# Kernel optimization log

Measured on AMD Instinct MI355X. Metric: run time of the kernel, lower is better.

## Reference

```python
import jax, jax.numpy as jnp
import numpy as np

D_STATE = 16
D_CONV = 4

def layernorm(x, g, b, eps=1e-5):
    m = jnp.mean(x, -1, keepdims=True)
    v = jnp.var(x, -1, keepdims=True)
    return (x - m) / jnp.sqrt(v + eps) * g + b

def conv1x1(x, w):  # x [b,h,w,cin], w [cin,cout]
    return jnp.einsum('bhwc,cd->bhwd', x, w)

def dwconv3x3(x, w):  # x [b,h,w,C], w [3,3,1,C] (HWIO, groups=C)
    return jax.lax.conv_general_dilated(x, w, (1, 1), 'SAME',
        dimension_numbers=('NHWC', 'HWIO', 'NHWC'),
        feature_group_count=x.shape[-1])

def causal_dwconv1d(x, w, b):  # x [B,L,D], w [K,1,D]; causal depthwise conv (Mamba d_conv=4)
    xp = jnp.pad(x, ((0, 0), (D_CONV - 1, 0), (0, 0)))
    y = jax.lax.conv_general_dilated(xp, w, (1,), 'VALID',
        dimension_numbers=('NWC', 'WIO', 'NWC'),
        feature_group_count=x.shape[-1])
    return y + b

def selective_scan(deltaA, deltaBx, C):
    # deltaA, deltaBx: [B,L,D,S]; C: [B,L,S] -> y: [B,L,D]
    def step(h, inp):
        dA, dBx, c = inp
        h = dA * h + dBx
        return h, jnp.einsum('bds,bs->bd', h, c)
    h0 = jnp.zeros(deltaA.shape[:1] + deltaA.shape[2:], deltaA.dtype)
    _, ys = jax.lax.scan(step, h0,
        (jnp.swapaxes(deltaA, 0, 1), jnp.swapaxes(deltaBx, 0, 1), jnp.swapaxes(C, 0, 1)))
    return jnp.swapaxes(ys, 0, 1)

def spa_ssm(x, in_w, conv_w, conv_b, xproj_w, dt_w, dt_b, Alog, D, out_w):
    # Mamba (slow path) applied to flattened spatial sequence; x: [b,h,w,c]
    b, h, w, c = x.shape
    L = h * w
    xs = x.reshape(b, L, c)
    di = Alog.shape[0]
    xz = xs @ in_w                       # [b,L,2*di]
    xi, z = xz[..., :di], xz[..., di:]
    xi = jax.nn.silu(causal_dwconv1d(xi, conv_w, conv_b))
    dbc = xi @ xproj_w                   # [b,L,dt_rank+2*S]
    dtr = dt_w.shape[0]
    dt = jax.nn.softplus(dbc[..., :dtr] @ dt_w + dt_b)   # [b,L,di]
    B = dbc[..., dtr:dtr + D_STATE]
    C = dbc[..., dtr + D_STATE:]
    A = -jnp.exp(Alog)                   # [di,S]
    deltaA = jnp.exp(dt[..., None] * A)                  # [b,L,di,S]
    deltaBx = (dt * xi)[..., None] * B[:, :, None, :]    # [b,L,di,S]
    y = selective_scan(deltaA, deltaBx, C) + D * xi
    y = y * jax.nn.silu(z)
    return (y @ out_w).reshape(b, h, w, c)

def camba_forward(x, ln1_g, ln1_b, vin_w1, vin_dw, vin_w2, vout_dw1, vout_dw2,
                  ssm_in_w, ssm_conv_w, ssm_conv_b, ssm_xproj_w, ssm_dt_w, ssm_dt_b,
                  ssm_Alog, ssm_D, ssm_out_w, ln2_g, ln2_b, ff_w1, ff_dw, ff_w2):
    x = jnp.transpose(x, (0, 2, 3, 1))   # [b,h,w,c]
    # ESSM: v_in_head = LN -> 1x1 -> dw3x3 -> GELU -> 1x1
    x0 = conv1x1(layernorm(x, ln1_g, ln1_b), vin_w1)
    x0 = jax.nn.gelu(dwconv3x3(x0, vin_dw), approximate=False)
    x0 = conv1x1(x0, vin_w2)
    y = spa_ssm(x0, ssm_in_w, ssm_conv_w, ssm_conv_b, ssm_xproj_w,
                ssm_dt_w, ssm_dt_b, ssm_Alog, ssm_D, ssm_out_w) + x0
    # v_out_head = dw3x3 -> GELU -> dw3x3, residual
    y = dwconv3x3(jax.nn.gelu(dwconv3x3(y, vout_dw1), approximate=False), vout_dw2) + y
    x = y + x                            # block residual
    # PreNorm FeedForward (mult=4): 1x1 -> LReLU -> dw3x3 -> LReLU -> 1x1
    t = layernorm(x, ln2_g, ln2_b)
    t = jax.nn.leaky_relu(conv1x1(t, ff_w1), 0.2)
    t = jax.nn.leaky_relu(dwconv3x3(t, ff_dw), 0.2)
    t = conv1x1(t, ff_w2)
    x = t + x
    return jnp.transpose(x, (0, 3, 1, 2))

def setup_inputs() -> dict:
    key = jax.random.key(0)
    ks = jax.random.split(key, 16)
    b, c, h, w = 8, 64, 64, 64
    di, ds, dtr = 128, 16, 4
    s = 0.05
    n = lambda k, shp: jax.random.normal(k, shp, jnp.float32) * s
    dt0 = jnp.exp(jax.random.uniform(ks[1], (di,)) * (np.log(0.1) - np.log(1e-3)) + np.log(1e-3))
    return dict(
        x=jax.random.normal(ks[0], (b, c, h, w), jnp.float32),
        ln1_g=jnp.ones(c), ln1_b=jnp.zeros(c),
        vin_w1=n(ks[2], (c, c)), vin_dw=n(ks[3], (3, 3, 1, c)), vin_w2=n(ks[4], (c, c)),
        vout_dw1=n(ks[5], (3, 3, 1, c)), vout_dw2=n(ks[6], (3, 3, 1, c)),
        ssm_in_w=n(ks[7], (c, 2 * di)),
        ssm_conv_w=n(ks[8], (D_CONV, 1, di)), ssm_conv_b=jnp.zeros(di),
        ssm_xproj_w=n(ks[9], (di, dtr + 2 * ds)),
        ssm_dt_w=n(ks[10], (dtr, di)), ssm_dt_b=jnp.log(jnp.expm1(dt0)),
        ssm_Alog=jnp.log(jnp.broadcast_to(jnp.arange(1., ds + 1), (di, ds))),
        ssm_D=jnp.ones(di),
        ssm_out_w=n(ks[11], (di, c)),
        ln2_g=jnp.ones(c), ln2_b=jnp.zeros(c),
        ff_w1=n(ks[12], (c, 4 * c)), ff_dw=n(ks[13], (3, 3, 1, 4 * c)), ff_w2=n(ks[14], (4 * c, c)),
    )

def reference(x, ln1_g, ln1_b, vin_w1, vin_dw, vin_w2, vout_dw1, vout_dw2,
              ssm_in_w, ssm_conv_w, ssm_conv_b, ssm_xproj_w, ssm_dt_w, ssm_dt_b,
              ssm_Alog, ssm_D, ssm_out_w, ln2_g, ln2_b, ff_w1, ff_dw, ff_w2):
    return camba_forward(x, ln1_g, ln1_b, vin_w1, vin_dw, vin_w2, vout_dw1, vout_dw2,
                         ssm_in_w, ssm_conv_w, ssm_conv_b, ssm_xproj_w, ssm_dt_w, ssm_dt_b,
                         ssm_Alog, ssm_D, ssm_out_w, ln2_g, ln2_b, ff_w1, ff_dw, ff_w2)
```

## Files before the change

### kernel.cpp

```cpp
#include <hip/hip_runtime.h>
#include <hip/hip_bf16.h>
#include <math.h>

typedef unsigned short u16;
typedef __attribute__((ext_vector_type(8))) short s8v;
typedef __attribute__((ext_vector_type(4))) float f4v;

#define B_    8
#define C_    64
#define HW_   4096
#define NPIX  32768
#define DI    128
#define NCH   256
#define CHL   16

__device__ __forceinline__ float b2f(u16 v){ return __uint_as_float(((unsigned)v)<<16); }
__device__ __forceinline__ u16 f2b(float x){
  unsigned u = __float_as_uint(x);
  u += 0x7fff + ((u >> 16) & 1);
  return (u16)(u >> 16);
}
__device__ __forceinline__ float gelu_exact(float x){ return 0.5f*x*(1.0f+erff(x*0.70710678118654752f)); }
__device__ __forceinline__ float leaky02(float x){ return x>0.f ? x : 0.2f*x; }
__device__ __forceinline__ float softplus_(float x){ return fmaxf(x,0.f)+log1pf(__expf(-fabsf(x))); }
__device__ __forceinline__ float silu_(float x){ return x / (1.0f + __expf(-x)); }
__device__ __forceinline__ void unpack16(uint4 q0, uint4 q1, float* v){
  unsigned w[8]={q0.x,q0.y,q0.z,q0.w,q1.x,q1.y,q1.z,q1.w};
  #pragma unroll
  for(int j=0;j<8;j++){
    v[2*j]   = __uint_as_float(w[j]<<16);
    v[2*j+1] = __uint_as_float(w[j]&0xffff0000u);
  }
}

__global__ void k_prep(const float* __restrict__ vin_w1, const float* __restrict__ vin_w2,
                       const float* __restrict__ ssm_in_w, const float* __restrict__ xproj,
                       const float* __restrict__ dtw, const float* __restrict__ ssm_outw,
                       const float* __restrict__ ff_w1, const float* __restrict__ ff_w2,
                       u16* __restrict__ wv1, u16* __restrict__ wv2, u16* __restrict__ wsi,
                       u16* __restrict__ wdb, u16* __restrict__ wout, u16* __restrict__ wf1,
                       u16* __restrict__ wf2t){
  int g = blockIdx.x*256 + threadIdx.x;
  if(g < 4096){
    int n=g>>6, c=g&63;
    wv1[n*64+c]=f2b(vin_w1[c*64+n]);
    wv2[n*64+c]=f2b(vin_w2[c*64+n]);
  }
  if(g < 16384){
    int n=g>>6, c=g&63;
    wsi[n*64+c]=f2b(ssm_in_w[c*256+n]);
    wf1[n*64+c]=f2b(ff_w1[c*256+n]);
    int n2=g/256, k2=g%256;
    wf2t[n2*256+k2]=f2b(ff_w2[k2*64+n2]);
  }
  if(g < 8192){
    int n=g>>7, k=g&127;
    wout[n*128+k]=f2b(ssm_outw[k*64+n]);
  }
  if(g < 20480){
    int n=g/128, k=g%128;
    float v;
    if(n < 128){
      v = 0.f;
      for(int r=0;r<4;r++) v += xproj[k*36+r]*dtw[r*128+n];
    }else{
      v = xproj[k*36+4+(n-128)];
    }
    wdb[n*128+k]=f2b(v);
  }
}

__global__ __launch_bounds__(256) void k_trans_ln_mm(const float* __restrict__ x,
                     const float* __restrict__ g, const float* __restrict__ bta,
                     const u16* __restrict__ wT,
                     u16* __restrict__ xT, u16* __restrict__ outp){
  const int LDA = 72, NS = 4;
  __shared__ float tile[64][65];
  __shared__ __align__(16) u16 sA[64*LDA];
  __shared__ __align__(16) u16 sW[64*LDA];
  int tid = threadIdx.x;
  int blk = blockIdx.x;
  int b = blk >> 6;
  int hwb = (blk & 63) << 6;
  int lane = tid & 63, row = tid >> 6;
  const float* src = x + (size_t)b*C_*HW_;
  #pragma unroll
  for(int k=0;k<16;k++){
    int c = row + 4*k;
    tile[c][lane] = src[c*HW_ + hwb + lane];
  }
  for(int idx=tid; idx<64*8; idx+=256){
    int n = idx>>3, c8 = (idx&7)*8;
    *(uint4*)(sW + n*LDA + c8) = *(const uint4*)(wT + n*64 + c8);
  }
  __syncthreads();
  u16* dstT = xT + (size_t)b*HW_*C_;
  #pragma unroll
  for(int k=0;k<16;k++){
    int hwl = row + 4*k;
    dstT[(hwb+hwl)*C_ + lane] = f2b(tile[lane][hwl]);
  }
  float gg = g[lane], bb = bta[lane];
  #pragma unroll
  for(int i=0;i<16;i++){
    int hwl = row*16 + i;
    float v = tile[lane][hwl];
    float s = v, sq = v*v;
    #pragma unroll
    for(int o=32;o>0;o>>=1){ s += __shfl_xor(s,o); sq += __shfl_xor(sq,o); }
    float m = s*(1.f/64.f);
    float var = sq*(1.f/64.f) - m*m;
    float r = rsqrtf(var + 1e-5f);
    sA[hwl*LDA + lane] = f2b((v-m)*r*gg + bb);
  }
  __syncthreads();
  int ln = tid & 63, wv = tid >> 6;
  int mrow = ln & 15, quad = ln >> 4;
  f4v acc[NS];
  #pragma unroll
  for(int i=0;i<NS;i++) acc[i] = (f4v){0.f,0.f,0.f,0.f};
  const u16* aBase = sA + (wv*16 + mrow)*LDA + quad*8;
  const u16* wBase = sW + mrow*LDA + quad*8;
  #pragma unroll
  for(int kk=0; kk<64; kk+=32){
    s8v af = *(const s8v*)(aBase + kk);
    #pragma unroll
    for(int ns=0; ns<NS; ns++){
      s8v bf = *(const s8v*)(wBase + ns*16*LDA + kk);
      acc[ns] = __builtin_amdgcn_mfma_f32_16x16x32_bf16(af, bf, acc[ns], 0, 0, 0);
    }
  }
  int p0 = blk*64;
  int pr = p0 + wv*16 + quad*4;
  #pragma unroll
  for(int ns=0; ns<NS; ns++){
    int n = ns*16 + mrow;
    #pragma unroll
    for(int r=0;r<4;r++)
      outp[(size_t)(pr+r)*64 + n] = f2b(acc[ns][r]);
  }
}

__global__ __launch_bounds__(256) void k_dw3mm(const u16* __restrict__ in,
                     const float* __restrict__ dwgt, const u16* __restrict__ wT,
                     u16* __restrict__ x0){
  const int LDT = 72;
  __shared__ __align__(16) u16 sIn[10*10*64];
  __shared__ __align__(16) u16 sT[64*LDT];
  __shared__ __align__(16) u16 sW[64*LDT];
  int tid = threadIdx.x;
  int blk = blockIdx.x;
  int b = blk >> 6;
  int t6 = blk & 63;
  int h0 = (t6 >> 3) * 8, w0 = (t6 & 7) * 8;
  for(int idx=tid; idx<64*8; idx+=256){
    int n = idx>>3, c8 = (idx&7)*8;
    *(uint4*)(sW + n*LDT + c8) = *(const uint4*)(wT + n*64 + c8);
  }
  for(int q=tid; q<10*10*16; q+=256){
    int pp = q >> 4, c4 = q & 15;
    int hh = pp / 10, ww = pp % 10;
    int gh = h0-1+hh, gw = w0-1+ww;
    ushort4 v = make_ushort4(0,0,0,0);
    if((unsigned)gh < 64u && (unsigned)gw < 64u)
      v = *(const ushort4*)(in + (size_t)((b*64+gh)*64+gw)*64 + c4*4);
    *(ushort4*)(sIn + pp*64 + c4*4) = v;
  }
  __syncthreads();
  int c4 = tid & 15;
  #pragma unroll
  for(int pass=0; pass<4; pass++){
    int opix = pass*16 + (tid>>4);
    int oh = opix >> 3, ow = opix & 7;
    float a0=0.f,a1=0.f,a2=0.f,a3=0.f;
    #pragma unroll
    for(int kh=0;kh<3;kh++){
      #pragma unroll
      for(int kw=0;kw<3;kw++){
        ushort4 v = *(const ushort4*)(sIn + ((oh+kh)*10 + (ow+kw))*64 + c4*4);
        float4 wv = *(const float4*)(dwgt + (kh*3+kw)*64 + c4*4);
        a0 += b2f(v.x)*wv.x; a1 += b2f(v.y)*wv.y;
        a2 += b2f(v.z)*wv.z; a3 += b2f(v.w)*wv.w;
      }
    }
    ushort4 o; o.x=f2b(gelu_exact(a0)); o.y=f2b(gelu_exact(a1));
    o.z=f2b(gelu_exact(a2)); o.w=f2b(gelu_exact(a3));
    *(ushort4*)(sT + opix*LDT + c4*4) = o;
  }
  __syncthreads();
  int ln = tid & 63, wv = tid >> 6;
  int mrow = ln & 15, quad = ln >> 4;
  f4v acc[4];
  #pragma unroll
  for(int i=0;i<4;i++) acc[i] = (f4v){0.f,0.f,0.f,0.f};
  const u16* aBase = sT + (wv*16 + mrow)*LDT + quad*8;
  const u16* wBase = sW + mrow*LDT + quad*8;
  #pragma unroll
  for(int kk=0; kk<64; kk+=32){
    s8v af = *(const s8v*)(aBase + kk);
    #pragma unroll
    for(int ns=0; ns<4; ns++){
      s8v bf = *(const s8v*)(wBase + ns*16*LDT + kk);
      acc[ns] = __builtin_amdgcn_mfma_f32_16x16x32_bf16(af, bf, acc[ns], 0, 0, 0);
    }
  }
  #pragma unroll
  for(int ns=0; ns<4; ns++){
    int n = ns*16 + mrow;
    #pragma unroll
    for(int r=0;r<4;r++){
      int opix = wv*16 + quad*4 + r;
      int oh = opix >> 3, ow = opix & 7;
      size_t p = ((size_t)(b*64 + h0+oh)*64 + (w0+ow));
      x0[p*64 + n] = f2b(acc[ns][r]);
    }
  }
}

template<int CIN, int COUT, int ACT, bool OUTF32>
__global__ __launch_bounds__(256) void k_mfma(const u16* __restrict__ wT,
                     const u16* __restrict__ in, const float* __restrict__ bias,
                     const u16* __restrict__ res, void* __restrict__ outv){
  const int KCH = (CIN < 128) ? CIN : 128;
  const int LDA = KCH + 8;
  const int NS  = COUT / 16;
  __shared__ __align__(16) u16 sA[64*LDA];
  __shared__ __align__(16) u16 sW[COUT*LDA];
  int tid = threadIdx.x;
  int p0 = blockIdx.x * 64;
  int ln = tid & 63, wv = tid >> 6;
  int mrow = ln & 15, quad = ln >> 4;
  f4v acc[NS];
  #pragma unroll
  for(int i=0;i<NS;i++) acc[i] = (f4v){0.f,0.f,0.f,0.f};
  const u16* aBase = sA + (wv*16 + mrow)*LDA + quad*8;
  const u16* wBase = sW + mrow*LDA + quad*8;
  const int RW = KCH/8;
  for(int k0=0; k0<CIN; k0+=KCH){
    if(k0) __syncthreads();
    for(int idx=tid; idx<COUT*RW; idx+=256){
      int n = idx/RW, c8 = (idx%RW)*8;
      *(uint4*)(sW + n*LDA + c8) = *(const uint4*)(wT + (size_t)n*CIN + k0 + c8);
    }
    for(int g=tid; g<64*RW; g+=256){
      int row = g / RW, c8 = (g % RW)*8;
      *(uint4*)(sA + row*LDA + c8) = *(const uint4*)(in + (size_t)(p0+row)*CIN + k0 + c8);
    }
    __syncthreads();
    #pragma unroll
    for(int kk=0; kk<KCH; kk+=32){
      s8v af = *(const s8v*)(aBase + kk);
      #pragma unroll
      for(int ns=0; ns<NS; ns++){
        s8v bf = *(const s8v*)(wBase + ns*16*LDA + kk);
        acc[ns] = __builtin_amdgcn_mfma_f32_16x16x32_bf16(af, bf, acc[ns], 0, 0, 0);
      }
    }
  }
  int pr = p0 + wv*16 + quad*4;
  #pragma unroll
  for(int ns=0; ns<NS; ns++){
    int n = ns*16 + mrow;
    float bs = bias ? bias[n] : 0.f;
    #pragma unroll
    for(int r=0;r<4;r++){
      float v = acc[ns][r] + bs;
      if(ACT==1) v = leaky02(v);
      else if(ACT==2) v = softplus_(v);
      if(res) v += b2f(res[(size_t)(pr+r)*COUT + n]);
      if(OUTF32) ((float*)outv)[(size_t)(pr+r)*COUT + n] = v;
      else       ((u16*)outv)[(size_t)(pr+r)*COUT + n] = f2b(v);
    }
  }
}

__global__ __launch_bounds__(256) void k_ssm_dtbc(const u16* __restrict__ wT,
                     const u16* __restrict__ x0,
                     const float* __restrict__ cw, const float* __restrict__ cb,
                     const u16* __restrict__ wdb, const float* __restrict__ dtbias,
                     u16* __restrict__ xi, u16* __restrict__ zs,
                     u16* __restrict__ dtout, u16* __restrict__ bcout){
  const int LDA=72, NS=16, LDY=136, LDWD=136, NS2=10;
  __shared__ __align__(16) u16 S[31616];
  u16* sW   = S;
  u16* sA   = S + 18432;
  u16* ubuf = S + 23040;
  u16* xiT  = S;
  u16* wdbS = S + 8704;
  int tid = threadIdx.x;
  int p0 = blockIdx.x*64;
  int ln = tid & 63, wv = tid >> 6;
  int mrow = ln & 15, quad = ln >> 4;
  for(int idx=tid; idx<256*8; idx+=256){
    int n = idx>>3, c8 = (idx&7)*8;
    *(uint4*)(sW + n*LDA + c8) = *(const uint4*)(wT + n*64 + c8);
  }
  for(int g=tid; g<64*8; g+=256){
    int row = g >> 3, c8 = (g & 7)*8;
    *(uint4*)(sA + row*LDA + c8) = *(const uint4*)(x0 + (size_t)(p0+row)*64 + c8);
  }
  __syncthreads();
  f4v acc[NS];
  #pragma unroll
  for(int i=0;i<NS;i++) acc[i] = (f4v){0.f,0.f,0.f,0.f};
  const u16* aBase = sA + (wv*16 + mrow)*LDA + quad*8;
  const u16* wBase = sW + mrow*LDA + quad*8;
  #pragma unroll
  for(int kk=0; kk<64; kk+=32){
    s8v af = *(const s8v*)(aBase + kk);
    #pragma unroll
    for(int ns=0; ns<NS; ns++){
      s8v bf = *(const s8v*)(wBase + ns*16*LDA + kk);
      acc[ns] = __builtin_amdgcn_mfma_f32_16x16x32_bf16(af, bf, acc[ns], 0, 0, 0);
    }
  }
  bool bstart = ((p0 & 4095) == 0);
  for(int idx=tid; idx<384; idx+=256){
    int j = idx >> 7, n = idx & 127;
    float a2 = 0.f;
    if(!bstart){
      const u16* xr = x0 + (size_t)(p0-3+j)*64;
      #pragma unroll 8
      for(int c=0;c<64;c++) a2 += b2f(xr[c]) * b2f(sW[n*LDA+c]);
    }
    ubuf[j*128 + n] = f2b(a2);
  }
  int prl = wv*16 + quad*4;
  #pragma unroll
  for(int ns=0; ns<NS; ns++){
    int n = ns*16 + mrow;
    if(n < 128){
      #pragma unroll
      for(int r=0;r<4;r++) ubuf[(prl+r+3)*128 + n] = f2b(acc[ns][r]);
    }else{
      #pragma unroll
      for(int r=0;r<4;r++) zs[(size_t)(p0+prl+r)*128 + (n-128)] = f2b(silu_(acc[ns][r]));
    }
  }
  __syncthreads();
  int d4 = tid & 31;
  float4 cbv = *(const float4*)(cb + d4*4);
  for(int row = tid >> 5; row < 64; row += 8){
    float a0=cbv.x, a1=cbv.y, a2=cbv.z, a3=cbv.w;
    #pragma unroll
    for(int k=0;k<4;k++){
      ushort4 v = *(const ushort4*)(ubuf + (row+k)*128 + d4*4);
      float4 wv4 = *(const float4*)(cw + k*128 + d4*4);
      a0 += b2f(v.x)*wv4.x; a1 += b2f(v.y)*wv4.y;
      a2 += b2f(v.z)*wv4.z; a3 += b2f(v.w)*wv4.w;
    }
    ushort4 o; o.x=f2b(silu_(a0)); o.y=f2b(silu_(a1)); o.z=f2b(silu_(a2)); o.w=f2b(silu_(a3));
    *(ushort4*)(xi + (size_t)(p0+row)*128 + d4*4) = o;
    *(ushort4*)(xiT + row*LDY + d4*4) = o;
  }
  __syncthreads();
  for(int idx=tid; idx<160*16; idx+=256){
    int n = idx>>4, c8 = (idx&15)*8;
    *(uint4*)(wdbS + n*LDWD + c8) = *(const uint4*)(wdb + n*128 + c8);
  }
  __syncthreads();
  f4v acc2[NS2];
  #pragma unroll
  for(int i=0;i<NS2;i++) acc2[i] = (f4v){0.f,0.f,0.f,0.f};
  #pragma unroll
  for(int kk=0; kk<128; kk+=32){
    s8v af = *(const s8v*)(xiT + (wv*16+mrow)*LDY + kk + quad*8);
    #pragma unroll
    for(int ns=0; ns<NS2; ns++){
      s8v bf = *(const s8v*)(wdbS + (ns*16+mrow)*LDWD + kk + quad*8);
      acc2[ns] = __builtin_amdgcn_mfma_f32_16x16x32_bf16(af, bf, acc2[ns], 0, 0, 0);
    }
  }
  int pr = p0 + wv*16 + quad*4;
  #pragma unroll
  for(int ns=0; ns<NS2; ns++){
    int n = ns*16 + mrow;
    if(n < 128){
      float bs = dtbias[n];
      #pragma unroll
      for(int r=0;r<4;r++)
        dtout[(size_t)(pr+r)*128 + n] = f2b(softplus_(acc2[ns][r] + bs));
    }else{
      #pragma unroll
      for(int r=0;r<4;r++)
        bcout[(size_t)(pr+r)*32 + (n-128)] = f2b(acc2[ns][r]);
    }
  }
}

__global__ __launch_bounds__(256) void k_scan1(const u16* __restrict__ dt, const u16* __restrict__ xi,
                        const u16* __restrict__ bc, const float* __restrict__ alog,
                        u16* __restrict__ Pb, u16* __restrict__ Qb){
  int t = blockIdx.x*256 + threadIdx.x;
  int d = t & 127;
  int ch = (t >> 7) & 255;
  int b = t >> 15;
  int pbase = b*HW_ + ch*CHL;
  float A[16];
  #pragma unroll
  for(int s=0;s<16;s++) A[s] = -__expf(alog[d*16+s]);
  float dtv[16], uv[16];
  #pragma unroll
  for(int i=0;i<CHL;i++){
    dtv[i] = b2f(dt[(size_t)(pbase+i)*128 + d]);
    uv[i]  = dtv[i] * b2f(xi[(size_t)(pbase+i)*128 + d]);
  }
  float Q[16], sumdt = 0.f;
  #pragma unroll
  for(int s=0;s<16;s++) Q[s] = 0.f;
  #pragma unroll
  for(int i=0;i<CHL;i++){
    float Bv[16];
    unpack16(*(const uint4*)(bc + (size_t)(pbase+i)*32),
             *(const uint4*)(bc + (size_t)(pbase+i)*32 + 8), Bv);
    sumdt += dtv[i];
    #pragma unroll
    for(int s=0;s<16;s++){
      float a = __expf(dtv[i]*A[s]);
      Q[s] = a*Q[s] + uv[i]*Bv[s];
    }
  }
  int gidx = ch*16384 + (b*128+d)*16;
  unsigned pw[8], qw[8];
  #pragma unroll
  for(int j=0;j<8;j++){
    pw[j] = (unsigned)f2b(__expf(A[2*j]*sumdt)) | ((unsigned)f2b(__expf(A[2*j+1]*sumdt))<<16);
    qw[j] = (unsigned)f2b(Q[2*j]) | ((unsigned)f2b(Q[2*j+1])<<16);
  }
  *(uint4*)(Pb+gidx)   = make_uint4(pw[0],pw[1],pw[2],pw[3]);
  *(uint4*)(Pb+gidx+8) = make_uint4(pw[4],pw[5],pw[6],pw[7]);
  *(uint4*)(Qb+gidx)   = make_uint4(qw[0],qw[1],qw[2],qw[3]);
  *(uint4*)(Qb+gidx+8) = make_uint4(qw[4],qw[5],qw[6],qw[7]);
}

__global__ __launch_bounds__(256) void k_scan2(const u16* __restrict__ Pb, const u16* __restrict__ Qb,
                        u16* __restrict__ Hin){
  __shared__ __align__(16) u16 sP[256*32];
  __shared__ __align__(16) u16 sQ[256*32];
  __shared__ float gP[8*32];
  __shared__ float gQ[8*32];
  int tid = threadIdx.x;
  int s0 = blockIdx.x * 32;
  for(int idx = tid; idx < 256*4; idx += 256){
    int ch = idx >> 2, j8 = (idx & 3) * 8;
    *(uint4*)(sP + ch*32 + j8) = *(const uint4*)(Pb + (size_t)ch*16384 + s0 + j8);
    *(uint4*)(sQ + ch*32 + j8) = *(const uint4*)(Qb + (size_t)ch*16384 + s0 + j8);
  }
  __syncthreads();
  int sl = tid & 31, grp = tid >> 5;
  int base = grp * 32;
  float P = 1.f, Q = 0.f;
  #pragma unroll 8
  for(int c = 0; c < 32; c++){
    float p = b2f(sP[(base+c)*32 + sl]);
    float q = b2f(sQ[(base+c)*32 + sl]);
    P = p * P;
    Q = p * Q + q;
  }
  gP[grp*32 + sl] = P;
  gQ[grp*32 + sl] = Q;
  __syncthreads();
  float h = 0.f;
  #pragma unroll
  for(int g = 0; g < 7; g++){
    if(g < grp) h = gP[g*32 + sl] * h + gQ[g*32 + sl];
  }
  for(int c = 0; c < 32; c++){
    Hin[(size_t)(base+c)*16384 + s0 + sl] = f2b(h);
    float p = b2f(sP[(base+c)*32 + sl]);
    float q = b2f(sQ[(base+c)*32 + sl]);
    h = p * h + q;
  }
}

__global__ __launch_bounds__(128) void k_scan3_mm(const u16* __restrict__ dt, const u16* __restrict__ xi,
                        const u16* __restrict__ bc, const u16* __restrict__ zs,
                        const float* __restrict__ alog, const float* __restrict__ Dp,
                        const u16* __restrict__ Hin, const u16* __restrict__ wout,
                        const u16* __restrict__ x0, u16* __restrict__ y){
  const int LDY = 136, LDW = 136;
  int blk = blockIdx.x;
  int ch = blk & (NCH-1);
  int b = blk >> 8;
  int d = threadIdx.x, tid = threadIdx.x;
  __shared__ __align__(16) u16 sY[CHL*LDY];
  __shared__ __align__(16) u16 sWo[64*LDW];
  __shared__ __align__(16) u16 sbc[CHL*32];
  for(int idx=tid; idx<64*16; idx+=128){
    int n = idx>>4, c8 = (idx&15)*8;
    *(uint4*)(sWo + n*LDW + c8) = *(const uint4*)(wout + n*128 + c8);
  }
  int pbase = b*HW_ + ch*CHL;
  if(tid < 64) ((uint4*)sbc)[tid] = ((const uint4*)(bc + (size_t)pbase*32))[tid];
  float A[16], h[16];
  u16 hbuf[16];
  int gidx = ch*16384 + (b*128+d)*16;
  *(uint4*)hbuf     = *(const uint4*)(Hin+gidx);
  *(uint4*)(hbuf+8) = *(const uint4*)(Hin+gidx+8);
  #pragma unroll
  for(int s=0;s<16;s++){ A[s] = -__expf(alog[d*16+s]); h[s] = b2f(hbuf[s]); }
  float Dd = Dp[d];
  float dtv[16], xiv[16], zsv[16];
  #pragma unroll
  for(int i=0;i<CHL;i++){
    dtv[i] = b2f(dt[(size_t)(pbase+i)*128 + d]);
    xiv[i] = b2f(xi[(size_t)(pbase+i)*128 + d]);
    zsv[i] = b2f(zs[(size_t)(pbase+i)*128 + d]);
  }
  __syncthreads();
  #pragma unroll
  for(int i=0;i<CHL;i++){
    float Bv[16], Cv[16];
    unpack16(*(const uint4*)(sbc + i*32),      *(const uint4*)(sbc + i*32 + 8),  Bv);
    unpack16(*(const uint4*)(sbc + i*32 + 16), *(const uint4*)(sbc + i*32 + 24), Cv);
    float u = dtv[i]*xiv[i];
    float acc = Dd*xiv[i];
    #pragma unroll
    for(int s=0;s<16;s++){
      float a = __expf(dtv[i]*A[s]);
      h[s] = a*h[s] + u*Bv[s];
      acc += h[s]*Cv[s];
    }
    sY[i*LDY + d] = f2b(acc * zsv[i]);
  }
  __syncthreads();
  int ln = tid & 63, wv = tid >> 6;
  int mrow = ln & 15, quad = ln >> 4;
  f4v acc2[2];
  acc2[0] = (f4v){0.f,0.f,0.f,0.f};
  acc2[1] = (f4v){0.f,0.f,0.f,0.f};
  #pragma unroll
  for(int kk=0; kk<128; kk+=32){
    s8v af = *(const s8v*)(sY + mrow*LDY + kk + quad*8);
    #pragma unroll
    for(int ns=0; ns<2; ns++){
      int n0 = wv*32 + ns*16;
      s8v bf = *(const s8v*)(sWo + (n0+mrow)*LDW + kk + quad*8);
      acc2[ns] = __builtin_amdgcn_mfma_f32_16x16x32_bf16(af, bf, acc2[ns], 0, 0, 0);
    }
  }
  #pragma unroll
  for(int ns=0; ns<2; ns++){
    int n = wv*32 + ns*16 + mrow;
    #pragma unroll
    for(int r=0;r<4;r++){
      int px = pbase + quad*4 + r;
      y[(size_t)px*64 + n] = f2b(acc2[ns][r] + b2f(x0[(size_t)px*64 + n]));
    }
  }
}

template<int COUT, int ACT>
__global__ __launch_bounds__(256) void k_mfma_ln(const u16* __restrict__ wT,
                     const u16* __restrict__ in, const float* __restrict__ g,
                     const float* __restrict__ bta, u16* __restrict__ outp){
  const int CIN = 64, LDA = 72, NS = COUT/16;
  __shared__ __align__(16) u16 sA[64*LDA];
  __shared__ __align__(16) u16 sW[COUT*LDA];
  int tid = threadIdx.x;
  int p0 = blockIdx.x * 64;
  int ln = tid & 63, wv = tid >> 6;
  int mrow = ln & 15, quad = ln >> 4;
  for(int idx=tid; idx<COUT*8; idx+=256){
    int n = idx>>3, c8 = (idx&7)*8;
    *(uint4*)(sW + n*LDA + c8) = *(const uint4*)(wT + n*64 + c8);
  }
  float gg = g[ln], bb = bta[ln];
  #pragma unroll
  for(int i=0;i<16;i++){
    int row = wv*16 + i;
    float v = b2f(in[(size_t)(p0+row)*64 + ln]);
    float s = v, sq = v*v;
    #pragma unroll
    for(int o=32;o>0;o>>=1){ s += __shfl_xor(s,o); sq += __shfl_xor(sq,o); }
    float m = s*(1.f/64.f);
    float var = sq*(1.f/64.f) - m*m;
    float r = rsqrtf(var + 1e-5f);
    sA[row*LDA + ln] = f2b((v-m)*r*gg + bb);
  }
  __syncthreads();
  f4v acc[NS];
  #pragma unroll
  for(int i=0;i<NS;i++) acc[i] = (f4v){0.f,0.f,0.f,0.f};
  const u16* aBase = sA + (wv*16 + mrow)*LDA + quad*8;
  const u16* wBase = sW + mrow*LDA + quad*8;
  #pragma unroll
  for(int kk=0; kk<CIN; kk+=32){
    s8v af = *(const s8v*)(aBase + kk);
    #pragma unroll
    for(int ns=0; ns<NS; ns++){
      s8v bf = *(const s8v*)(wBase + ns*16*LDA + kk);
      acc[ns] = __builtin_amdgcn_mfma_f32_16x16x32_bf16(af, bf, acc[ns], 0, 0, 0);
    }
  }
  int pr = p0 + wv*16 + quad*4;
  #pragma unroll
  for(int ns=0; ns<NS; ns++){
    int n = ns*16 + mrow;
    #pragma unroll
    for(int r=0;r<4;r++){
      float v = acc[ns][r];
      if(ACT==1) v = leaky02(v);
      outp[(size_t)(pr+r)*COUT + n] = f2b(v);
    }
  }
}

__global__ __launch_bounds__(256) void k_mfma_fin(const u16* __restrict__ wT,
                     const u16* __restrict__ in, const u16* __restrict__ res,
                     float* __restrict__ outp){
  const int CIN=256, COUT=64, KCH=128, LDA=136, NS=4;
  __shared__ __align__(16) u16 sA[64*LDA];
  __shared__ __align__(16) u16 sW[COUT*LDA];
  int tid = threadIdx.x;
  int p0 = blockIdx.x * 64;
  int ln = tid & 63, wv = tid >> 6;
  int mrow = ln & 15, quad = ln >> 4;
  f4v acc[NS];
  #pragma unroll
  for(int i=0;i<NS;i++) acc[i] = (f4v){0.f,0.f,0.f,0.f};
  const u16* aBase = sA + (wv*16 + mrow)*LDA + quad*8;
  const u16* wBase = sW + mrow*LDA + quad*8;
  for(int k0=0; k0<CIN; k0+=KCH){
    if(k0) __syncthreads();
    for(int idx=tid; idx<COUT*16; idx+=256){
      int n = idx>>4, c8 = (idx&15)*8;
      *(uint4*)(sW + n*LDA + c8) = *(const uint4*)(wT + n*256 + k0 + c8);
    }
    for(int g=tid; g<64*16; g+=256){
      int row = g >> 4, c8 = (g & 15)*8;
      *(uint4*)(sA + row*LDA + c8) = *(const uint4*)(in + (size_t)(p0+row)*CIN + k0 + c8);
    }
    __syncthreads();
    #pragma unroll
    for(int kk=0; kk<KCH; kk+=32){
      s8v af = *(const s8v*)(aBase + kk);
      #pragma unroll
      for(int ns=0; ns<NS; ns++){
        s8v bf = *(const s8v*)(wBase + ns*16*LDA + kk);
        acc[ns] = __builtin_amdgcn_mfma_f32_16x16x32_bf16(af, bf, acc[ns], 0, 0, 0);
      }
    }
  }
  int pr = p0 + wv*16 + quad*4;
  int b = blockIdx.x >> 6;
  int hwr = ((blockIdx.x & 63) << 6) + wv*16 + quad*4;
  #pragma unroll
  for(int ns=0; ns<NS; ns++){
    int n = ns*16 + mrow;
    float4 v4;
    v4.x = acc[ns][0] + b2f(res[(size_t)(pr+0)*64 + n]);
    v4.y = acc[ns][1] + b2f(res[(size_t)(pr+1)*64 + n]);
    v4.z = acc[ns][2] + b2f(res[(size_t)(pr+2)*64 + n]);
    v4.w = acc[ns][3] + b2f(res[(size_t)(pr+3)*64 + n]);
    *(float4*)(outp + (size_t)b*C_*HW_ + (size_t)n*HW_ + hwr) = v4;
  }
}

__global__ __launch_bounds__(256) void k_dw3x2(const u16* __restrict__ yin,
                      const float* __restrict__ w1, const float* __restrict__ w2,
                      const u16* __restrict__ xTr, u16* __restrict__ outp){
  const int LDH = 68;
  __shared__ __align__(16) u16 sY[144*LDH];
  __shared__ __align__(16) u16 sT[100*LDH];
  int tid = threadIdx.x;
  int blk = blockIdx.x;
  int b = blk >> 6;
  int t6 = blk & 63;
  int h0 = (t6 >> 3) * 8, w0 = (t6 & 7) * 8;
  for(int q=tid; q<144*16; q+=256){
    int pp = q >> 4, c4 = q & 15;
    int hh = pp / 12, ww = pp - hh*12;
    int gh = h0-2+hh, gw = w0-2+ww;
    ushort4 v = make_ushort4(0,0,0,0);
    if((unsigned)gh < 64u && (unsigned)gw < 64u)
      v = *(const ushort4*)(yin + (size_t)((b*64+gh)*64+gw)*64 + c4*4);
    *(ushort4*)(sY + pp*LDH + c4*4) = v;
  }
  __syncthreads();
  int c4 = tid & 15;
  #pragma unroll
  for(int pass=0; pass<7; pass++){
    int tpix = pass*16 + (tid>>4);
    if(tpix < 100){
      int th = tpix / 10, tw = tpix - th*10;
      int gh = h0-1+th, gw = w0-1+tw;
      ushort4 o = make_ushort4(0,0,0,0);
      if((unsigned)gh < 64u && (unsigned)gw < 64u){
        float a0=0.f,a1=0.f,a2=0.f,a3=0.f;
        #pragma unroll
        for(int kh=0;kh<3;kh++){
          #pragma unroll
          for(int kw=0;kw<3;kw++){
            ushort4 v = *(const ushort4*)(sY + ((th+kh)*12 + (tw+kw))*LDH + c4*4);
            float4 wv = *(const float4*)(w1 + (kh*3+kw)*64 + c4*4);
            a0 += b2f(v.x)*wv.x; a1 += b2f(v.y)*wv.y;
            a2 += b2f(v.z)*wv.z; a3 += b2f(v.w)*wv.w;
          }
        }
        o.x=f2b(gelu_exact(a0)); o.y=f2b(gelu_exact(a1));
        o.z=f2b(gelu_exact(a2)); o.w=f2b(gelu_exact(a3));
      }
      *(ushort4*)(sT + tpix*LDH + c4*4) = o;
    }
  }
  __syncthreads();
  #pragma unroll
  for(int pass=0; pass<4; pass++){
    int opix = pass*16 + (tid>>4);
    int oh = opix >> 3, ow = opix & 7;
    float a0=0.f,a1=0.f,a2=0.f,a3=0.f;
    #pragma unroll
    for(int kh=0;kh<3;kh++){
      #pragma unroll
      for(int kw=0;kw<3;kw++){
        ushort4 v = *(const ushort4*)(sT + ((oh+kh)*10 + (ow+kw))*LDH + c4*4);
        float4 wv = *(const float4*)(w2 + (kh*3+kw)*64 + c4*4);
        a0 += b2f(v.x)*wv.x; a1 += b2f(v.y)*wv.y;
        a2 += b2f(v.z)*wv.z; a3 += b2f(v.w)*wv.w;
      }
    }
    size_t gp = (size_t)((b*64 + h0+oh)*64 + (w0+ow));
    ushort4 ry = *(const ushort4*)(sY + ((oh+2)*12 + (ow+2))*LDH + c4*4);
    ushort4 rx = *(const ushort4*)(xTr + gp*64 + c4*4);
    a0 += b2f(ry.x); a0 += b2f(rx.x);
    a1 += b2f(ry.y); a1 += b2f(rx.y);
    a2 += b2f(ry.z); a2 += b2f(rx.z);
    a3 += b2f(ry.w); a3 += b2f(rx.w);
    ushort4 o; o.x=f2b(a0); o.y=f2b(a1); o.z=f2b(a2); o.w=f2b(a3);
    *(ushort4*)(outp + gp*64 + c4*4) = o;
  }
}

template<int CN, int ACT>
__global__ void k_dw3(const u16* __restrict__ in, const float* __restrict__ wgt,
                      const u16* __restrict__ res1, const u16* __restrict__ res2,
                      u16* __restrict__ out){
  const int C4 = CN/4;
  int g = blockIdx.x*256 + threadIdx.x;
  int c4 = g % C4;
  int pix = g / C4;
  int w = pix & 63;
  int h = (pix >> 6) & 63;
  int b = pix >> 12;
  float a0=0.f, a1=0.f, a2=0.f, a3=0.f;
  #pragma unroll
  for(int kh=0;kh<3;kh++){
    int hh = h + kh - 1;
    if((unsigned)hh < 64u){
      #pragma unroll
      for(int kw=0;kw<3;kw++){
        int ww = w + kw - 1;
        if((unsigned)ww < 64u){
          ushort4 v = *(const ushort4*)(in + (size_t)((b*64+hh)*64 + ww)*CN + c4*4);
          float4 wv = *(const float4*)(wgt + (kh*3+kw)*CN + c4*4);
          a0 += b2f(v.x)*wv.x; a1 += b2f(v.y)*wv.y;
          a2 += b2f(v.z)*wv.z; a3 += b2f(v.w)*wv.w;
        }
      }
    }
  }
  if(ACT==1){ a0=leaky02(a0); a1=leaky02(a1); a2=leaky02(a2); a3=leaky02(a3); }
  else if(ACT==2){ a0=gelu_exact(a0); a1=gelu_exact(a1); a2=gelu_exact(a2); a3=gelu_exact(a3); }
  size_t ob = (size_t)pix*CN + c4*4;
  if(res1){ ushort4 r = *(const ushort4*)(res1 + ob);
            a0+=b2f(r.x); a1+=b2f(r.y); a2+=b2f(r.z); a3+=b2f(r.w); }
  if(res2){ ushort4 r = *(const ushort4*)(res2 + ob);
            a0+=b2f(r.x); a1+=b2f(r.y); a2+=b2f(r.z); a3+=b2f(r.w); }
  ushort4 o; o.x=f2b(a0); o.y=f2b(a1); o.z=f2b(a2); o.w=f2b(a3);
  *(ushort4*)(out + ob) = o;
}

extern "C" void kernel_launch(void* const* d_in, const int* in_sizes, int n_in,
                              void* d_out, int out_size, void* d_ws, size_t ws_size,
                              hipStream_t stream) {
  const float* x        = (const float*)d_in[0];
  const float* ln1_g    = (const float*)d_in[1];
  const float* ln1_b    = (const float*)d_in[2];
  const float* vin_w1   = (const float*)d_in[3];
  const float* vin_dw   = (const float*)d_in[4];
  const float* vin_w2   = (const float*)d_in[5];
  const float* vout_dw1 = (const float*)d_in[6];
  const float* vout_dw2 = (const float*)d_in[7];
  const float* ssm_in_w = (const float*)d_in[8];
  const float* ssm_cw   = (const float*)d_in[9];
  const float* ssm_cb   = (const float*)d_in[10];
  const float* ssm_xprj = (const float*)d_in[11];
  const float* ssm_dtw  = (const float*)d_in[12];
  const float* ssm_dtb  = (const float*)d_in[13];
  const float* ssm_Alog = (const float*)d_in[14];
  const float* ssm_D    = (const float*)d_in[15];
  const float* ssm_outw = (const float*)d_in[16];
  const float* ln2_g    = (const float*)d_in[17];
  const float* ln2_b    = (const float*)d_in[18];
  const float* ff_w1    = (const float*)d_in[19];
  const float* ff_dw    = (const float*)d_in[20];
  const float* ff_w2    = (const float*)d_in[21];
  float* out = (float*)d_out;

  const size_t M = 1u<<20;
  u16* U   = (u16*)d_ws;
  u16* xT  = U;
  u16* tA  = U + 2*M;
  u16* tB  = U + 4*M;
  u16* x0  = U + 6*M;
  u16* xi  = U + 8*M;
  u16* zs  = U + 12*M;
  u16* xz  = U + 16*M;
  u16* dtb = U + 24*M;
  u16* bc  = U + 28*M;
  u16* Pb  = U + 16*M;
  u16* Qb  = U + 20*M;
  u16* Hin = tA;
  u16* y   = U + 16*M;
  u16* t2  = dtb;
  u16* wv1  = U + 33*M;
  u16* wv2  = wv1 + 4096;
  u16* wsi  = wv2 + 4096;
  u16* wdb  = wsi + 16384;
  u16* wout = wdb + 20480;
  u16* wf1  = wout + 8192;
  u16* wf2t = wf1 + 16384;

  k_prep<<<80,256,0,stream>>>(vin_w1, vin_w2, ssm_in_w, ssm_xprj, ssm_dtw, ssm_outw,
                              ff_w1, ff_w2, wv1, wv2, wsi, wdb, wout, wf1, wf2t);

  k_trans_ln_mm<<<512,256,0,stream>>>(x, ln1_g, ln1_b, wv1, xT, tB);
  k_dw3mm<<<512,256,0,stream>>>(tB, vin_dw, wv2, x0);

  k_ssm_dtbc<<<512,256,0,stream>>>(wsi, x0, ssm_cw, ssm_cb, wdb, ssm_dtb,
                                   xi, zs, dtb, bc);
  k_scan1<<<1024,256,0,stream>>>(dtb, xi, bc, ssm_Alog, Pb, Qb);
  k_scan2<<<512,256,0,stream>>>(Pb, Qb, Hin);
  k_scan3_mm<<<2048,128,0,stream>>>(dtb, xi, bc, zs, ssm_Alog, ssm_D, Hin, wout, x0, y);

  k_dw3x2<<<512,256,0,stream>>>(y, vout_dw1, vout_dw2, xT, x0);

  k_mfma_ln<256,1><<<512,256,0,stream>>>(wf1, x0, ln2_g, ln2_b, xz);
  k_dw3<256,1><<<8192,256,0,stream>>>(xz, ff_dw, nullptr, nullptr, t2);
  k_mfma_fin<<<512,256,0,stream>>>(wf2t, t2, x0, out);
}
```

Before: 261.2 us.

## Fuse FFN LayerNorm, 1x1 expand, depthwise 3x3, and 1x1 project into one kernel

Replaces the three FFN kernels (LN+expand GEMM, depthwise 3x3 conv, project GEMM+residual) with one tiled kernel per 8x8 spatial tile. Each block normalises a 10x10 halo tile into LDS, computes the expanded 256-channel activations in 64-channel chunks, applies the depthwise conv from LDS, and accumulates the projection in registers. This removes the global round trips of the 4x-wide intermediate tensors. In exchange it recomputes the expansion GEMM on halo pixels and runs more serial work per block under heavier LDS use.

```diff
diff --git a/kernel.cpp b/kernel.cpp
--- a/kernel.cpp
+++ b/kernel.cpp
@@ -213,63 +213,6 @@
       int oh = opix >> 3, ow = opix & 7;
       size_t p = ((size_t)(b*64 + h0+oh)*64 + (w0+ow));
       x0[p*64 + n] = f2b(acc[ns][r]);
-    }
-  }
-}
-
-template<int CIN, int COUT, int ACT, bool OUTF32>
-__global__ __launch_bounds__(256) void k_mfma(const u16* __restrict__ wT,
-                     const u16* __restrict__ in, const float* __restrict__ bias,
-                     const u16* __restrict__ res, void* __restrict__ outv){
-  const int KCH = (CIN < 128) ? CIN : 128;
-  const int LDA = KCH + 8;
-  const int NS  = COUT / 16;
-  __shared__ __align__(16) u16 sA[64*LDA];
-  __shared__ __align__(16) u16 sW[COUT*LDA];
-  int tid = threadIdx.x;
-  int p0 = blockIdx.x * 64;
-  int ln = tid & 63, wv = tid >> 6;
-  int mrow = ln & 15, quad = ln >> 4;
-  f4v acc[NS];
-  #pragma unroll
-  for(int i=0;i<NS;i++) acc[i] = (f4v){0.f,0.f,0.f,0.f};
-  const u16* aBase = sA + (wv*16 + mrow)*LDA + quad*8;
-  const u16* wBase = sW + mrow*LDA + quad*8;
-  const int RW = KCH/8;
-  for(int k0=0; k0<CIN; k0+=KCH){
-    if(k0) __syncthreads();
-    for(int idx=tid; idx<COUT*RW; idx+=256){
-      int n = idx/RW, c8 = (idx%RW)*8;
-      *(uint4*)(sW + n*LDA + c8) = *(const uint4*)(wT + (size_t)n*CIN + k0 + c8);
-    }
-    for(int g=tid; g<64*RW; g+=256){
-      int row = g / RW, c8 = (g % RW)*8;
-      *(uint4*)(sA + row*LDA + c8) = *(const uint4*)(in + (size_t)(p0+row)*CIN + k0 + c8);
-    }
-    __syncthreads();
-    #pragma unroll
-    for(int kk=0; kk<KCH; kk+=32){
-      s8v af = *(const s8v*)(aBase + kk);
-      #pragma unroll
-      for(int ns=0; ns<NS; ns++){
-        s8v bf = *(const s8v*)(wBase + ns*16*LDA + kk);
-        acc[ns] = __builtin_amdgcn_mfma_f32_16x16x32_bf16(af, bf, acc[ns], 0, 0, 0);
-      }
-    }
-  }
-  int pr = p0 + wv*16 + quad*4;
-  #pragma unroll
-  for(int ns=0; ns<NS; ns++){
-    int n = ns*16 + mrow;
-    float bs = bias ? bias[n] : 0.f;
-    #pragma unroll
-    for(int r=0;r<4;r++){
-      float v = acc[ns][r] + bs;
-      if(ACT==1) v = leaky02(v);
-      else if(ACT==2) v = softplus_(v);
-      if(res) v += b2f(res[(size_t)(pr+r)*COUT + n]);
-      if(OUTF32) ((float*)outv)[(size_t)(pr+r)*COUT + n] = v;
-      else       ((u16*)outv)[(size_t)(pr+r)*COUT + n] = f2b(v);
     }
   }
 }
@@ -547,113 +490,6 @@
       int px = pbase + quad*4 + r;
       y[(size_t)px*64 + n] = f2b(acc2[ns][r] + b2f(x0[(size_t)px*64 + n]));
     }
-  }
-}
-
-template<int COUT, int ACT>
-__global__ __launch_bounds__(256) void k_mfma_ln(const u16* __restrict__ wT,
-                     const u16* __restrict__ in, const float* __restrict__ g,
-                     const float* __restrict__ bta, u16* __restrict__ outp){
-  const int CIN = 64, LDA = 72, NS = COUT/16;
-  __shared__ __align__(16) u16 sA[64*LDA];
-  __shared__ __align__(16) u16 sW[COUT*LDA];
-  int tid = threadIdx.x;
-  int p0 = blockIdx.x * 64;
-  int ln = tid & 63, wv = tid >> 6;
-  int mrow = ln & 15, quad = ln >> 4;
-  for(int idx=tid; idx<COUT*8; idx+=256){
-    int n = idx>>3, c8 = (idx&7)*8;
-    *(uint4*)(sW + n*LDA + c8) = *(const uint4*)(wT + n*64 + c8);
-  }
-  float gg = g[ln], bb = bta[ln];
-  #pragma unroll
-  for(int i=0;i<16;i++){
-    int row = wv*16 + i;
-    float v = b2f(in[(size_t)(p0+row)*64 + ln]);
-    float s = v, sq = v*v;
-    #pragma unroll
-    for(int o=32;o>0;o>>=1){ s += __shfl_xor(s,o); sq += __shfl_xor(sq,o); }
-    float m = s*(1.f/64.f);
-    float var = sq*(1.f/64.f) - m*m;
-    float r = rsqrtf(var + 1e-5f);
-    sA[row*LDA + ln] = f2b((v-m)*r*gg + bb);
-  }
-  __syncthreads();
-  f4v acc[NS];
-  #pragma unroll
-  for(int i=0;i<NS;i++) acc[i] = (f4v){0.f,0.f,0.f,0.f};
-  const u16* aBase = sA + (wv*16 + mrow)*LDA + quad*8;
-  const u16* wBase = sW + mrow*LDA + quad*8;
-  #pragma unroll
-  for(int kk=0; kk<CIN; kk+=32){
-    s8v af = *(const s8v*)(aBase + kk);
-    #pragma unroll
-    for(int ns=0; ns<NS; ns++){
-      s8v bf = *(const s8v*)(wBase + ns*16*LDA + kk);
-      acc[ns] = __builtin_amdgcn_mfma_f32_16x16x32_bf16(af, bf, acc[ns], 0, 0, 0);
-    }
-  }
-  int pr = p0 + wv*16 + quad*4;
-  #pragma unroll
-  for(int ns=0; ns<NS; ns++){
-    int n = ns*16 + mrow;
-    #pragma unroll
-    for(int r=0;r<4;r++){
-      float v = acc[ns][r];
-      if(ACT==1) v = leaky02(v);
-      outp[(size_t)(pr+r)*COUT + n] = f2b(v);
-    }
-  }
-}
-
-__global__ __launch_bounds__(256) void k_mfma_fin(const u16* __restrict__ wT,
-                     const u16* __restrict__ in, const u16* __restrict__ res,
-                     float* __restrict__ outp){
-  const int CIN=256, COUT=64, KCH=128, LDA=136, NS=4;
-  __shared__ __align__(16) u16 sA[64*LDA];
-  __shared__ __align__(16) u16 sW[COUT*LDA];
-  int tid = threadIdx.x;
-  int p0 = blockIdx.x * 64;
-  int ln = tid & 63, wv = tid >> 6;
-  int mrow = ln & 15, quad = ln >> 4;
-  f4v acc[NS];
-  #pragma unroll
-  for(int i=0;i<NS;i++) acc[i] = (f4v){0.f,0.f,0.f,0.f};
-  const u16* aBase = sA + (wv*16 + mrow)*LDA + quad*8;
-  const u16* wBase = sW + mrow*LDA + quad*8;
-  for(int k0=0; k0<CIN; k0+=KCH){
-    if(k0) __syncthreads();
-    for(int idx=tid; idx<COUT*16; idx+=256){
-      int n = idx>>4, c8 = (idx&15)*8;
-      *(uint4*)(sW + n*LDA + c8) = *(const uint4*)(wT + n*256 + k0 + c8);
-    }
-    for(int g=tid; g<64*16; g+=256){
-      int row = g >> 4, c8 = (g & 15)*8;
-      *(uint4*)(sA + row*LDA + c8) = *(const uint4*)(in + (size_t)(p0+row)*CIN + k0 + c8);
-    }
-    __syncthreads();
-    #pragma unroll
-    for(int kk=0; kk<KCH; kk+=32){
-      s8v af = *(const s8v*)(aBase + kk);
-      #pragma unroll
-      for(int ns=0; ns<NS; ns++){
-        s8v bf = *(const s8v*)(wBase + ns*16*LDA + kk);
-        acc[ns] = __builtin_amdgcn_mfma_f32_16x16x32_bf16(af, bf, acc[ns], 0, 0, 0);
-      }
-    }
-  }
-  int pr = p0 + wv*16 + quad*4;
-  int b = blockIdx.x >> 6;
-  int hwr = ((blockIdx.x & 63) << 6) + wv*16 + quad*4;
-  #pragma unroll
-  for(int ns=0; ns<NS; ns++){
-    int n = ns*16 + mrow;
-    float4 v4;
-    v4.x = acc[ns][0] + b2f(res[(size_t)(pr+0)*64 + n]);
-    v4.y = acc[ns][1] + b2f(res[(size_t)(pr+1)*64 + n]);
-    v4.z = acc[ns][2] + b2f(res[(size_t)(pr+2)*64 + n]);
-    v4.w = acc[ns][3] + b2f(res[(size_t)(pr+3)*64 + n]);
-    *(float4*)(outp + (size_t)b*C_*HW_ + (size_t)n*HW_ + hwr) = v4;
   }
 }
 
@@ -732,43 +568,122 @@
   }
 }
 
-template<int CN, int ACT>
-__global__ void k_dw3(const u16* __restrict__ in, const float* __restrict__ wgt,
-                      const u16* __restrict__ res1, const u16* __restrict__ res2,
-                      u16* __restrict__ out){
-  const int C4 = CN/4;
-  int g = blockIdx.x*256 + threadIdx.x;
-  int c4 = g % C4;
-  int pix = g / C4;
-  int w = pix & 63;
-  int h = (pix >> 6) & 63;
-  int b = pix >> 12;
-  float a0=0.f, a1=0.f, a2=0.f, a3=0.f;
-  #pragma unroll
-  for(int kh=0;kh<3;kh++){
-    int hh = h + kh - 1;
-    if((unsigned)hh < 64u){
-      #pragma unroll
-      for(int kw=0;kw<3;kw++){
-        int ww = w + kw - 1;
-        if((unsigned)ww < 64u){
-          ushort4 v = *(const ushort4*)(in + (size_t)((b*64+hh)*64 + ww)*CN + c4*4);
-          float4 wv = *(const float4*)(wgt + (kh*3+kw)*CN + c4*4);
-          a0 += b2f(v.x)*wv.x; a1 += b2f(v.y)*wv.y;
-          a2 += b2f(v.z)*wv.z; a3 += b2f(v.w)*wv.w;
+__global__ __launch_bounds__(256) void k_ffn(const u16* __restrict__ xR,
+                     const float* __restrict__ g, const float* __restrict__ bta,
+                     const u16* __restrict__ wf1, const u16* __restrict__ wf2t,
+                     const float* __restrict__ fdw, float* __restrict__ outp){
+  const int LDX = 72;
+  __shared__ __align__(16) u16 sX[112*LDX];
+  __shared__ __align__(16) u16 sT1[112*LDX];
+  __shared__ __align__(16) u16 sW1[64*LDX];
+  __shared__ __align__(16) u16 sW2[64*LDX];
+  __shared__ float sDW[9*256];
+  int tid = threadIdx.x;
+  int blk = blockIdx.x;
+  int b = blk >> 6;
+  int t6 = blk & 63;
+  int h0 = (t6 >> 3)*8, w0 = (t6 & 7)*8;
+  int ln = tid & 63, wv = tid >> 6;
+  int mrow = ln & 15, quad = ln >> 4;
+  for(int i=tid; i<9*64; i+=256) ((float4*)sDW)[i] = ((const float4*)fdw)[i];
+  float gg = g[ln], bb = bta[ln];
+  for(int hp = wv; hp < 112; hp += 4){
+    u16 o = 0;
+    if(hp < 100){
+      int th = hp/10, tw = hp - th*10;
+      int gh = h0-1+th, gw = w0-1+tw;
+      if((unsigned)gh < 64u && (unsigned)gw < 64u){
+        float v = b2f(xR[(size_t)((b*64+gh)*64+gw)*64 + ln]);
+        float s = v, sq = v*v;
+        #pragma unroll
+        for(int o2=32;o2>0;o2>>=1){ s += __shfl_xor(s,o2); sq += __shfl_xor(sq,o2); }
+        float m = s*(1.f/64.f);
+        float var = sq*(1.f/64.f) - m*m;
+        float r = rsqrtf(var + 1e-5f);
+        o = f2b((v-m)*r*gg + bb);
+      }
+    }
+    sX[hp*LDX + ln] = o;
+  }
+  f4v acc2[4];
+  #pragma unroll
+  for(int i=0;i<4;i++) acc2[i] = (f4v){0.f,0.f,0.f,0.f};
+  int p = wv*16 + mrow;
+  int oh = p >> 3, ow = p & 7;
+  for(int c=0; c<4; c++){
+    int nc0 = c*64;
+    __syncthreads();
+    for(int idx=tid; idx<64*8; idx+=256){
+      int n = idx>>3, c8 = (idx&7)*8;
+      *(uint4*)(sW1 + n*LDX + c8) = *(const uint4*)(wf1 + (size_t)(nc0+n)*64 + c8);
+      *(uint4*)(sW2 + n*LDX + c8) = *(const uint4*)(wf2t + (size_t)n*256 + nc0 + c8);
+    }
+    __syncthreads();
+    for(int mt = wv; mt < 7; mt += 4){
+      f4v a1[4];
+      #pragma unroll
+      for(int i=0;i<4;i++) a1[i] = (f4v){0.f,0.f,0.f,0.f};
+      const u16* aB = sX + (mt*16 + mrow)*LDX + quad*8;
+      const u16* wB = sW1 + mrow*LDX + quad*8;
+      #pragma unroll
+      for(int kk=0; kk<64; kk+=32){
+        s8v af = *(const s8v*)(aB + kk);
+        #pragma unroll
+        for(int ns=0; ns<4; ns++){
+          s8v bf = *(const s8v*)(wB + ns*16*LDX + kk);
+          a1[ns] = __builtin_amdgcn_mfma_f32_16x16x32_bf16(af, bf, a1[ns], 0, 0, 0);
         }
       }
-    }
-  }
-  if(ACT==1){ a0=leaky02(a0); a1=leaky02(a1); a2=leaky02(a2); a3=leaky02(a3); }
-  else if(ACT==2){ a0=gelu_exact(a0); a1=gelu_exact(a1); a2=gelu_exact(a2); a3=gelu_exact(a3); }
-  size_t ob = (size_t)pix*CN + c4*4;
-  if(res1){ ushort4 r = *(const ushort4*)(res1 + ob);
-            a0+=b2f(r.x); a1+=b2f(r.y); a2+=b2f(r.z); a3+=b2f(r.w); }
-  if(res2){ ushort4 r = *(const ushort4*)(res2 + ob);
-            a0+=b2f(r.x); a1+=b2f(r.y); a2+=b2f(r.z); a3+=b2f(r.w); }
-  ushort4 o; o.x=f2b(a0); o.y=f2b(a1); o.z=f2b(a2); o.w=f2b(a3);
-  *(ushort4*)(out + ob) = o;
+      #pragma unroll
+      for(int ns=0; ns<4; ns++)
+        #pragma unroll
+        for(int r=0; r<4; r++)
+          sT1[(mt*16 + quad*4 + r)*LDX + ns*16 + mrow] = f2b(leaky02(a1[ns][r]));
+    }
+    __syncthreads();
+    #pragma unroll
+    for(int half=0; half<2; half++){
+      int ch0 = half*32 + quad*8;
+      float a[8];
+      #pragma unroll
+      for(int j=0;j<8;j++) a[j] = 0.f;
+      #pragma unroll
+      for(int kh=0;kh<3;kh++){
+        #pragma unroll
+        for(int kw=0;kw<3;kw++){
+          s8v v = *(const s8v*)(sT1 + ((oh+kh)*10 + (ow+kw))*LDX + ch0);
+          const float* wp = sDW + (kh*3+kw)*256 + nc0 + ch0;
+          float4 w0v = *(const float4*)(wp);
+          float4 w1v = *(const float4*)(wp+4);
+          a[0] += b2f((u16)v[0])*w0v.x; a[1] += b2f((u16)v[1])*w0v.y;
+          a[2] += b2f((u16)v[2])*w0v.z; a[3] += b2f((u16)v[3])*w0v.w;
+          a[4] += b2f((u16)v[4])*w1v.x; a[5] += b2f((u16)v[5])*w1v.y;
+          a[6] += b2f((u16)v[6])*w1v.z; a[7] += b2f((u16)v[7])*w1v.w;
+        }
+      }
+      s8v af;
+      #pragma unroll
+      for(int j=0;j<8;j++) af[j] = (short)f2b(leaky02(a[j]));
+      #pragma unroll
+      for(int ns=0; ns<4; ns++){
+        s8v bf = *(const s8v*)(sW2 + (ns*16 + mrow)*LDX + half*32 + quad*8);
+        acc2[ns] = __builtin_amdgcn_mfma_f32_16x16x32_bf16(af, bf, acc2[ns], 0, 0, 0);
+      }
+    }
+  }
+  int pe = wv*16 + quad*4;
+  int eoh = pe >> 3, eow0 = pe & 7;
+  size_t gbase = (size_t)((b*64 + h0 + eoh)*64 + (w0 + eow0));
+  #pragma unroll
+  for(int ns=0; ns<4; ns++){
+    int n = ns*16 + mrow;
+    float4 v4;
+    v4.x = acc2[ns][0] + b2f(xR[(gbase+0)*64 + n]);
+    v4.y = acc2[ns][1] + b2f(xR[(gbase+1)*64 + n]);
+    v4.z = acc2[ns][2] + b2f(xR[(gbase+2)*64 + n]);
+    v4.w = acc2[ns][3] + b2f(xR[(gbase+3)*64 + n]);
+    *(float4*)(outp + (size_t)b*C_*HW_ + (size_t)n*HW_ + (h0+eoh)*64 + (w0+eow0)) = v4;
+  }
 }
 
 extern "C" void kernel_launch(void* const* d_in, const int* in_sizes, int n_in,
@@ -806,14 +721,12 @@
   u16* x0  = U + 6*M;
   u16* xi  = U + 8*M;
   u16* zs  = U + 12*M;
-  u16* xz  = U + 16*M;
   u16* dtb = U + 24*M;
   u16* bc  = U + 28*M;
   u16* Pb  = U + 16*M;
   u16* Qb  = U + 20*M;
   u16* Hin = tA;
   u16* y   = U + 16*M;
-  u16* t2  = dtb;
   u16* wv1  = U + 33*M;
   u16* wv2  = wv1 + 4096;
   u16* wsi  = wv2 + 4096;
@@ -836,7 +749,5 @@
 
   k_dw3x2<<<512,256,0,stream>>>(y, vout_dw1, vout_dw2, xT, x0);
 
-  k_mfma_ln<256,1><<<512,256,0,stream>>>(wf1, x0, ln2_g, ln2_b, xz);
-  k_dw3<256,1><<<8192,256,0,stream>>>(xz, ff_dw, nullptr, nullptr, t2);
-  k_mfma_fin<<<512,256,0,stream>>>(wf2t, t2, x0, out);
-}
+  k_ffn<<<512,256,0,stream>>>(x0, ln2_g, ln2_b, wf1, wf2t, ff_dw, out);
+}
```

New measurement: 247.1 us. 1.06x faster.
